# Kernel tuning notes

Measured on AMD Instinct MI355X. Metric: run time of the kernel, lower is better.

Reference implementation:

```python
import jax, jax.numpy as jnp
import numpy as np

FACTOR = 5  # init factor


def setup_inputs() -> dict:
    key = jax.random.key(0)
    k1, k2, k3, k4 = jax.random.split(key, 4)
    B, H, L, D = 4, 8, 2048, 64
    sample_k = min(FACTOR * int(np.ceil(np.log(L))), L)  # 40
    queries = jax.random.normal(k1, (B, H, L, D), dtype=jnp.float32)
    keys = jax.random.normal(k2, (B, H, L, D), dtype=jnp.float32)
    values = jax.random.normal(k3, (B, H, L, D), dtype=jnp.float32)
    index_sample = jax.random.randint(k4, (L, sample_k), 0, L)
    return {"queries": queries, "keys": keys, "values": values,
            "index_sample": index_sample}


def reference(queries, keys, values, index_sample):
    B, H, L_Q, D = queries.shape
    L_K = keys.shape[2]
    n_top = min(FACTOR * int(np.ceil(np.log(L_Q))), L_Q)

    # --- _prob_QK ---
    # Gather sampled keys per query position: [B,H,L_Q,sample_k,D]
    K_sample = keys[:, :, index_sample, :]
    # Q.unsqueeze(3) @ K_sample^T -> [B,H,L_Q,sample_k]
    Q_K_sample = jnp.einsum('bhld,bhlsd->bhls', queries, K_sample)
    # sparsity measure M = max - mean
    M = Q_K_sample.max(axis=-1) - Q_K_sample.sum(axis=-1) / L_K
    _, M_top = jax.lax.top_k(M, n_top)  # [B,H,n_top]
    # gather top queries: [B,H,n_top,D]
    Q_reduce = jnp.take_along_axis(queries, M_top[..., None], axis=2)
    # full scores for top queries: [B,H,n_top,L_K]
    scores_top = jnp.einsum('bhud,bhkd->bhuk', Q_reduce, keys)

    # --- scale ---
    scale = 1.0 / np.sqrt(D).astype(np.float32)
    scores_top = scores_top * scale

    # --- initial context (mask_flag=False): mean of V broadcast over L_Q ---
    V_mean = values.mean(axis=2)  # [B,H,D]
    context = jnp.broadcast_to(V_mean[:, :, None, :], (B, H, L_Q, D))

    # --- update context at top-query positions ---
    attn = jax.nn.softmax(scores_top, axis=-1)           # [B,H,n_top,L_K]
    ctx_update = jnp.einsum('bhuk,bhkd->bhud', attn, values)
    b_idx = jnp.arange(B)[:, None, None]
    h_idx = jnp.arange(H)[None, :, None]
    context = context.at[b_idx, h_idx, M_top].set(ctx_update)
    return context
```

## Files before the change

### kernel.cpp

```cpp
#include <hip/hip_runtime.h>
#include <math.h>

#define BH 32
#define L  2048
#define D  64
#define SK 40
#define NT 40
#define NC 32
#define CK 64
#define SP 65
#define SCALE 0.125f

#define WS_M      0
#define WS_MTOP   262144
#define WS_VP     267264
#define WS_VM     529408
#define WS_QTOP   537600
#define WS_OPART  865280
#define WS_MPART  11351040
#define WS_LPART  11514880

template <int CTRL>
__device__ __forceinline__ float dpp_add(float x) {
    int y = __builtin_amdgcn_update_dpp(0, __float_as_int(x), CTRL, 0xF, 0xF, true);
    return x + __int_as_float(y);
}

__global__ __launch_bounds__(512) void kMV(const float* __restrict__ Q,
                                           const float* __restrict__ K,
                                           const float* __restrict__ V,
                                           const int* __restrict__ idx,
                                           float* __restrict__ M,
                                           float* __restrict__ Vp)
{
    __shared__ int   sidx[64 * SK];
    __shared__ float red[512];

    int t    = threadIdx.x;
    int b    = blockIdx.x;
    int head = ((b >> 3) & 3) * 8 + (b & 7);
    int qc   = b >> 5;
    int l0   = qc * 64;

    {
        int d = t & 63, r = t >> 6;
        const float* Vb = V + ((size_t)head * L + l0 + r * 8) * D + d;
        float acc = 0.f;
        #pragma unroll
        for (int k = 0; k < 8; ++k) acc += Vb[(size_t)k * D];
        red[t] = acc;
    }
    for (int i = t; i < 64 * SK; i += 512) sidx[i] = idx[l0 * SK + i];
    __syncthreads();
    if (t < 64) {
        float s = 0.f;
        #pragma unroll
        for (int rr = 0; rr < 8; ++rr) s += red[t + rr * 64];
        Vp[(head * 32 + qc) * 64 + t] = s;
    }

    int wave = t >> 6, lane = t & 63;
    int g16  = lane >> 4;
    int dl   = lane & 15;

    const float4* Q4  = reinterpret_cast<const float4*>(Q);
    const float4* Kb4 = reinterpret_cast<const float4*>(K) + (size_t)head * L * 16;

    #pragma unroll
    for (int qr = 0; qr < 2; ++qr) {
        int lq = wave * 8 + qr * 4 + g16;
        size_t qid = (size_t)head * L + (l0 + lq);
        float4 q4 = Q4[qid * 16 + dl];

        float mx0 = -INFINITY, mx1 = -INFINITY, sm0 = 0.f, sm1 = 0.f;
        #pragma unroll 8
        for (int s = 0; s < SK; ++s) {
            int kr = sidx[lq * SK + s];
            float4 k4 = Kb4[(size_t)kr * 16 + dl];
            float p = q4.x * k4.x + q4.y * k4.y + q4.z * k4.z + q4.w * k4.w;
            p = dpp_add<0xB1>(p);
            p = dpp_add<0x4E>(p);
            p = dpp_add<0x12C>(p);
            p = dpp_add<0x128>(p);
            if (s & 1) { mx1 = fmaxf(mx1, p); sm1 += p; }
            else       { mx0 = fmaxf(mx0, p); sm0 += p; }
        }
        if (dl == 0) M[qid] = fmaxf(mx0, mx1) - (sm0 + sm1) * (1.0f / (float)L);
    }
}

__global__ __launch_bounds__(1024) void kTopVm(const float* __restrict__ M,
                                               const float* __restrict__ Vp,
                                               const float* __restrict__ Q,
                                               int* __restrict__ Mtop,
                                               float* __restrict__ Vm,
                                               float* __restrict__ Qtop)
{
    __shared__ unsigned int keys[L];
    __shared__ int hist[256];
    __shared__ int wtot[4];
    __shared__ unsigned int pref_s;
    __shared__ int krem_s;
    __shared__ int cnt_gt, cnt_eq;
    __shared__ int eqlist[64];
    __shared__ int stop[NT];

    int bh = blockIdx.x;
    int t  = threadIdx.x;
    int lane = t & 63, w = t >> 6;

    if (t < 64) {
        float s = 0.f;
        #pragma unroll
        for (int c = 0; c < 32; ++c) s += Vp[(bh * 32 + c) * 64 + t];
        Vm[bh * D + t] = s * (1.0f / (float)L);
    }

    for (int i = t; i < L; i += 1024) {
        unsigned int u = __float_as_uint(M[bh * L + i]);
        keys[i] = (u & 0x80000000u) ? ~u : (u | 0x80000000u);
    }
    if (t == 0) { pref_s = 0u; krem_s = NT; cnt_gt = 0; cnt_eq = 0; }
    __syncthreads();

    #pragma unroll
    for (int shift = 24; shift >= 0; shift -= 8) {
        if (t < 256) hist[t] = 0;
        __syncthreads();
        unsigned int pref = pref_s;
        int krem = krem_s;
        for (int i = t; i < L; i += 1024) {
            unsigned int k  = keys[i];
            unsigned int hi = (shift == 24) ? 0u : (k >> (shift + 8));
            if (hi == pref) atomicAdd(&hist[(k >> shift) & 0xFF], 1);
        }
        __syncthreads();
        int h = 0, v = 0;
        if (t < 256) {
            h = hist[t];
            v = h;
            #pragma unroll
            for (int o = 1; o < 64; o <<= 1) {
                int u = __shfl_down(v, o, 64);
                if (lane + o < 64) v += u;
            }
            if (lane == 0) wtot[w] = v;
        }
        __syncthreads();
        if (t < 256) {
            int ss = v;
            #pragma unroll
            for (int w2 = 1; w2 < 4; ++w2) if (w2 > w) ss += wtot[w2];
            if (ss - h < krem && ss >= krem) {
                krem_s = krem - (ss - h);
                pref_s = (pref << 8) | (unsigned int)t;
            }
        }
    }
    __syncthreads();

    unsigned int T = pref_s;
    int krem = krem_s;
    for (int i = t; i < L; i += 1024) {
        unsigned int k = keys[i];
        if (k > T) {
            int p = atomicAdd(&cnt_gt, 1);
            Mtop[bh * NT + p] = i;
            stop[p] = i;
        } else if (k == T) {
            int p = atomicAdd(&cnt_eq, 1);
            if (p < 64) eqlist[p] = i;
        }
    }
    __syncthreads();
    if (t == 0) {
        int base = cnt_gt;
        int m = cnt_eq < 64 ? cnt_eq : 64;
        for (int q = 0; q < krem; ++q) {
            int best = 0x7fffffff, bj = -1;
            for (int j = 0; j < m; ++j) if (eqlist[j] < best) { best = eqlist[j]; bj = j; }
            Mtop[bh * NT + base + q] = best;
            stop[base + q] = best;
            if (bj >= 0) eqlist[bj] = 0x7fffffff;
        }
    }
    __syncthreads();
    const float4* Qg = reinterpret_cast<const float4*>(Q) + (size_t)bh * L * 16;
    float4* Qt = reinterpret_cast<float4*>(Qtop) + (size_t)bh * NT * 16;
    for (int i = t; i < NT * 16; i += 1024)
        Qt[i] = Qg[(size_t)stop[i >> 4] * 16 + (i & 15)];
}

__global__ __launch_bounds__(256, 2) void kAttnPart(const float* __restrict__ Qtop,
                                                    const float* __restrict__ K,
                                                    const float* __restrict__ V,
                                                    const float* __restrict__ Vm,
                                                    float* __restrict__ Opart,
                                                    float* __restrict__ mpart,
                                                    float* __restrict__ lpart,
                                                    float* __restrict__ out)
{
    __shared__ float4 V4s[CK * 16];
    __shared__ float  S[NT * SP];
    __shared__ float  smax[NT], ssum[NT];

    int c = blockIdx.x, bh = blockIdx.y;
    int t = threadIdx.x;

    {
        const float4* Vm4 = reinterpret_cast<const float4*>(Vm + bh * D);
        float4* outB = reinterpret_cast<float4*>(out) + ((size_t)bh * L + c * CK) * 16;
        #pragma unroll
        for (int k = 0; k < 4; ++k) { int i = t + k * 256; outB[i] = Vm4[i & 15]; }
    }

    int w    = __builtin_amdgcn_readfirstlane(t) >> 6;
    int lane = t & 63;
    const float4* Kg = reinterpret_cast<const float4*>(K) + ((size_t)bh * L + c * CK) * 16;
    float4 k[16];
    #pragma unroll
    for (int d4 = 0; d4 < 16; ++d4) k[d4] = Kg[(size_t)lane * 16 + d4];

    const float4* Qb = reinterpret_cast<const float4*>(Qtop) + ((size_t)bh * NT + w * 10) * 16;
    float p[10];
    #pragma unroll
    for (int i = 0; i < 10; ++i) {
        float a0 = 0.f;
        #pragma unroll
        for (int d4 = 0; d4 < 16; ++d4) {
            float4 q4 = Qb[i * 16 + d4];
            a0 += q4.x * k[d4].x + q4.y * k[d4].y + q4.z * k[d4].z + q4.w * k[d4].w;
        }
        p[i] = a0 * SCALE;
    }

    #pragma unroll
    for (int i = 0; i < 10; ++i) {
        int u = w * 10 + i;
        float m = p[i];
        #pragma unroll
        for (int o = 1; o < 64; o <<= 1) m = fmaxf(m, __shfl_xor(m, o, 64));
        float e = __expf(p[i] - m);
        float l2 = e;
        #pragma unroll
        for (int o = 1; o < 64; o <<= 1) l2 += __shfl_xor(l2, o, 64);
        S[u * SP + lane] = e;
        if (lane == 0) { smax[u] = m; ssum[u] = l2; }
    }

    __builtin_amdgcn_sched_barrier(0);
    {
        const float4* Vg = reinterpret_cast<const float4*>(V) + ((size_t)bh * L + c * CK) * 16;
        float4 v0 = Vg[t];
        float4 v1 = Vg[t + 256];
        float4 v2 = Vg[t + 512];
        float4 v3 = Vg[t + 768];
        int i0 = t,       j0 = i0 >> 4, c0 = i0 & 15;
        int i1 = t + 256, j1 = i1 >> 4, c1 = i1 & 15;
        int i2 = t + 512, j2 = i2 >> 4, c2 = i2 & 15;
        int i3 = t + 768, j3 = i3 >> 4, c3 = i3 & 15;
        V4s[j0 * 16 + (c0 ^ (j0 & 15))] = v0;
        V4s[j1 * 16 + (c1 ^ (j1 & 15))] = v1;
        V4s[j2 * 16 + (c2 ^ (j2 & 15))] = v2;
        V4s[j3 * 16 + (c3 ^ (j3 & 15))] = v3;
    }
    __syncthreads();

    {
        int a = t >> 5, r = t & 31;
        int d4 = r >> 1, jh = r & 1;
        float4 acc[5];
        #pragma unroll
        for (int ui = 0; ui < 5; ++ui) acc[ui] = make_float4(0.f, 0.f, 0.f, 0.f);
        for (int jj = 0; jj < 32; ++jj) {
            int j = jh * 32 + jj;
            float4 v4 = V4s[j * 16 + (d4 ^ (j & 15))];
            #pragma unroll
            for (int ui = 0; ui < 5; ++ui) {
                float pw = S[(a + 8 * ui) * SP + j];
                acc[ui].x += pw * v4.x; acc[ui].y += pw * v4.y;
                acc[ui].z += pw * v4.z; acc[ui].w += pw * v4.w;
            }
        }
        #pragma unroll
        for (int ui = 0; ui < 5; ++ui) {
            acc[ui].x = dpp_add<0xB1>(acc[ui].x);
            acc[ui].y = dpp_add<0xB1>(acc[ui].y);
            acc[ui].z = dpp_add<0xB1>(acc[ui].z);
            acc[ui].w = dpp_add<0xB1>(acc[ui].w);
        }
        if (jh == 0) {
            float4* Og = reinterpret_cast<float4*>(Opart) + ((size_t)(bh * NC + c) * NT) * 16;
            #pragma unroll
            for (int ui = 0; ui < 5; ++ui)
                Og[(a + 8 * ui) * 16 + d4] = acc[ui];
        }
    }
    if (t < NT) {
        mpart[(bh * NC + c) * NT + t] = smax[t];
        lpart[(bh * NC + c) * NT + t] = ssum[t];
    }
}

__global__ __launch_bounds__(256) void kCombine(const float* __restrict__ Opart,
                                                const float* __restrict__ mpart,
                                                const float* __restrict__ lpart,
                                                const int* __restrict__ Mtop,
                                                float* __restrict__ out)
{
    int t = threadIdx.x, bh = blockIdx.y;
    int u = blockIdx.x * 4 + (t >> 6);
    int d = t & 63;
    float gm = -INFINITY;
    #pragma unroll
    for (int c = 0; c < NC; ++c) gm = fmaxf(gm, mpart[(bh * NC + c) * NT + u]);
    float den = 0.f, o = 0.f;
    #pragma unroll
    for (int c = 0; c < NC; ++c) {
        int pi = (bh * NC + c) * NT + u;
        float wgt = __expf(mpart[pi] - gm);
        den += wgt * lpart[pi];
        o   += wgt * Opart[(size_t)pi * D + d];
    }
    int qrow = Mtop[bh * NT + u];
    out[((size_t)bh * L + qrow) * D + d] = o / den;
}

extern "C" void kernel_launch(void* const* d_in, const int* in_sizes, int n_in,
                              void* d_out, int out_size, void* d_ws, size_t ws_size,
                              hipStream_t stream)
{
    const float* Q   = (const float*)d_in[0];
    const float* K   = (const float*)d_in[1];
    const float* V   = (const float*)d_in[2];
    const int*   idx = (const int*)d_in[3];
    float* out = (float*)d_out;

    char* ws = (char*)d_ws;
    float* M     = (float*)(ws + WS_M);
    int*   Mtop  = (int*)  (ws + WS_MTOP);
    float* Vp    = (float*)(ws + WS_VP);
    float* Vm    = (float*)(ws + WS_VM);
    float* Qtop  = (float*)(ws + WS_QTOP);
    float* Opart = (float*)(ws + WS_OPART);
    float* mpart = (float*)(ws + WS_MPART);
    float* lpart = (float*)(ws + WS_LPART);

    kMV      <<<1024, 512, 0, stream>>>(Q, K, V, idx, M, Vp);
    kTopVm   <<<BH, 1024, 0, stream>>>(M, Vp, Q, Mtop, Vm, Qtop);
    kAttnPart<<<dim3(NC, BH), 256, 0, stream>>>(Qtop, K, V, Vm, Opart, mpart, lpart, out);
    kCombine <<<dim3(NT / 4, BH), 256, 0, stream>>>(Opart, mpart, lpart, Mtop, out);
}
```

Before: 161.6 us.

## Fuse split-softmax combine into attention kernel via last-block atomic counter

Removes the separate combine kernel launch. Each attention block increments a per-head atomic counter after writing its partials, and the last block to arrive merges all 32 chunk partials for that head. The counter is reset in the top-k kernel. This saves one launch but serializes the combine onto a single block per head, which leaves much of the GPU idle at the tail. It also depends on threadfence and atomic ordering for correctness.

```diff
diff --git a/kernel.cpp b/kernel.cpp
--- a/kernel.cpp
+++ b/kernel.cpp
@@ -19,6 +19,7 @@
 #define WS_OPART  865280
 #define WS_MPART  11351040
 #define WS_LPART  11514880
+#define WS_CNT    11678720
 
 template <int CTRL>
 __device__ __forceinline__ float dpp_add(float x) {
@@ -94,7 +95,8 @@
                                                const float* __restrict__ Q,
                                                int* __restrict__ Mtop,
                                                float* __restrict__ Vm,
-                                               float* __restrict__ Qtop)
+                                               float* __restrict__ Qtop,
+                                               int* __restrict__ cnt)
 {
     __shared__ unsigned int keys[L];
     __shared__ int hist[256];
@@ -108,6 +110,8 @@
     int bh = blockIdx.x;
     int t  = threadIdx.x;
     int lane = t & 63, w = t >> 6;
+
+    if (t == 0) cnt[bh] = 0;
 
     if (t < 64) {
         float s = 0.f;
@@ -195,14 +199,17 @@
                                                     const float* __restrict__ K,
                                                     const float* __restrict__ V,
                                                     const float* __restrict__ Vm,
+                                                    const int* __restrict__ Mtop,
                                                     float* __restrict__ Opart,
                                                     float* __restrict__ mpart,
                                                     float* __restrict__ lpart,
+                                                    int* __restrict__ cnt,
                                                     float* __restrict__ out)
 {
     __shared__ float4 V4s[CK * 16];
     __shared__ float  S[NT * SP];
     __shared__ float  smax[NT], ssum[NT];
+    __shared__ int    gate;
 
     int c = blockIdx.x, bh = blockIdx.y;
     int t = threadIdx.x;
@@ -300,30 +307,36 @@
         mpart[(bh * NC + c) * NT + t] = smax[t];
         lpart[(bh * NC + c) * NT + t] = ssum[t];
     }
-}
-
-__global__ __launch_bounds__(256) void kCombine(const float* __restrict__ Opart,
-                                                const float* __restrict__ mpart,
-                                                const float* __restrict__ lpart,
-                                                const int* __restrict__ Mtop,
-                                                float* __restrict__ out)
-{
-    int t = threadIdx.x, bh = blockIdx.y;
-    int u = blockIdx.x * 4 + (t >> 6);
-    int d = t & 63;
-    float gm = -INFINITY;
-    #pragma unroll
-    for (int c = 0; c < NC; ++c) gm = fmaxf(gm, mpart[(bh * NC + c) * NT + u]);
-    float den = 0.f, o = 0.f;
-    #pragma unroll
-    for (int c = 0; c < NC; ++c) {
-        int pi = (bh * NC + c) * NT + u;
-        float wgt = __expf(mpart[pi] - gm);
-        den += wgt * lpart[pi];
-        o   += wgt * Opart[(size_t)pi * D + d];
-    }
-    int qrow = Mtop[bh * NT + u];
-    out[((size_t)bh * L + qrow) * D + d] = o / den;
+
+    __syncthreads();
+    if (t == 0) {
+        __threadfence();
+        gate = atomicAdd(&cnt[bh], 1);
+        __threadfence();
+    }
+    __syncthreads();
+    if (gate != NC - 1) return;
+
+    {
+        int u4 = t >> 6, d = t & 63;
+        #pragma unroll
+        for (int u0 = 0; u0 < 10; ++u0) {
+            int u = u0 * 4 + u4;
+            float gm = -INFINITY;
+            #pragma unroll
+            for (int cc = 0; cc < NC; ++cc) gm = fmaxf(gm, mpart[(bh * NC + cc) * NT + u]);
+            float den = 0.f, o = 0.f;
+            #pragma unroll
+            for (int cc = 0; cc < NC; ++cc) {
+                int pi = (bh * NC + cc) * NT + u;
+                float wgt = __expf(mpart[pi] - gm);
+                den += wgt * lpart[pi];
+                o   += wgt * Opart[(size_t)pi * D + d];
+            }
+            int qrow = Mtop[bh * NT + u];
+            out[((size_t)bh * L + qrow) * D + d] = o / den;
+        }
+    }
 }
 
 extern "C" void kernel_launch(void* const* d_in, const int* in_sizes, int n_in,
@@ -345,9 +358,10 @@
     float* Opart = (float*)(ws + WS_OPART);
     float* mpart = (float*)(ws + WS_MPART);
     float* lpart = (float*)(ws + WS_LPART);
+    int*   cnt   = (int*)  (ws + WS_CNT);
 
     kMV      <<<1024, 512, 0, stream>>>(Q, K, V, idx, M, Vp);
-    kTopVm   <<<BH, 1024, 0, stream>>>(M, Vp, Q, Mtop, Vm, Qtop);
-    kAttnPart<<<dim3(NC, BH), 256, 0, stream>>>(Qtop, K, V, Vm, Opart, mpart, lpart, out);
-    kCombine <<<dim3(NT / 4, BH), 256, 0, stream>>>(Opart, mpart, lpart, Mtop, out);
-}
+    kTopVm   <<<BH, 1024, 0, stream>>>(M, Vp, Q, Mtop, Vm, Qtop, cnt);
+    kAttnPart<<<dim3(NC, BH), 256, 0, stream>>>(Qtop, K, V, Vm, Mtop,
+                                                Opart, mpart, lpart, cnt, out);
+}
```

After: 261.9 us. 1.62x slower.
